# Optimization experiments

Measured on AMD Instinct MI355X. Metric: run time of the kernel, lower is better.

The kernel has to match this reference:

```python
import jax, jax.numpy as jnp
import numpy as np
import math

B, D, NH, NS, NT = 16, 256, 512, 8, 32
NV = NS * NT          # 256 prediction variables
L, H, A = 4, 8, 64    # attention layers, heads, head dim
HA = H * A            # 512
M = 512               # mlp_dim
R = 128               # resolution
EPS = 1e-5


def setup_inputs() -> dict:
    key = jax.random.key(0)
    ks = jax.random.split(key, 32)
    s = 0.02
    inp = {
        'hist_encoded': jax.random.normal(ks[0], (B, NH, D), jnp.float32),
        'hist_true_u': jax.random.uniform(ks[1], (B, NH), jnp.float32),
        'pred_encoded': jax.random.normal(ks[2], (B, NV, D), jnp.float32),
        'pred_true_u': jax.random.uniform(ks[3], (B, NV), jnp.float32),
        # dimension shifting layer
        'ds_w': jax.random.normal(ks[4], (D, HA), jnp.float32) * s,
        'ds_b': jnp.zeros((HA,), jnp.float32),
        # per-layer, per-head key/value creators: Linear(D+1 -> A)
        'key_w': jax.random.normal(ks[5], (L, H, D + 1, A), jnp.float32) * s,
        'key_b': jnp.zeros((L, H, A), jnp.float32),
        'val_w': jax.random.normal(ks[6], (L, H, D + 1, A), jnp.float32) * s,
        'val_b': jnp.zeros((L, H, A), jnp.float32),
        # layer norms
        'ln1_g': jnp.ones((L, HA), jnp.float32),
        'ln1_b': jnp.zeros((L, HA), jnp.float32),
        'ln2_g': jnp.ones((L, HA), jnp.float32),
        'ln2_b': jnp.zeros((L, HA), jnp.float32),
        # feed-forward (mlp_layers=2): HA->M, M->M, M->HA
        'ff_w1': jax.random.normal(ks[7], (L, HA, M), jnp.float32) * s,
        'ff_b1': jnp.zeros((L, M), jnp.float32),
        'ff_w2': jax.random.normal(ks[8], (L, M, M), jnp.float32) * s,
        'ff_b2': jnp.zeros((L, M), jnp.float32),
        'ff_w3': jax.random.normal(ks[9], (L, M, HA), jnp.float32) * s,
        'ff_b3': jnp.zeros((L, HA), jnp.float32),
        # dist extractor
        'de_w': jax.random.normal(ks[10], (HA, R), jnp.float32) * s,
        'de_b': jnp.zeros((R,), jnp.float32),
        'num_series': NS,
        'num_timesteps': NT,
    }
    return inp


def _ln(x, g, b):
    m = x.mean(-1, keepdims=True)
    v = ((x - m) ** 2).mean(-1, keepdims=True)
    return g * (x - m) / jnp.sqrt(v + EPS) + b


def _forward(hist_encoded, hist_true_u, pred_encoded, pred_true_u,
             ds_w, ds_b, key_w, key_b, val_w, val_b,
             ln1_g, ln1_b, ln2_g, ln2_b,
             ff_w1, ff_b1, ff_w2, ff_b2, ff_w3, ff_b3,
             de_w, de_b):
    Bm, NVm, Dm = pred_encoded.shape
    NHm = hist_encoded.shape[1]
    Lm, Hm, _, Am = key_w.shape
    W = NHm + NVm
    # identity permutation in the source loss() -> no-op
    att = pred_encoded @ ds_w + ds_b  # [B, NV, HA]
    # key/value inputs: [hist||u ; pred||u] -> [B, W, D+1]
    ki = jnp.concatenate([
        jnp.concatenate([hist_encoded, hist_true_u[:, :, None]], axis=2),
        jnp.concatenate([pred_encoded, pred_true_u[:, :, None]], axis=2)], axis=1)
    keys = jnp.einsum('bwd,lhda->lbhwa', ki, key_w) + key_b[:, None, :, None, :]
    vals = jnp.einsum('bwd,lhda->lbhwa', ki, val_w) + val_b[:, None, :, None, :]
    # flipped-triangular mask: position w is masked iff w >= NH + v
    mask = jnp.arange(W)[None, :] >= (NHm + jnp.arange(NVm)[:, None])  # [NV, W]
    scale = Am ** (-0.5)
    for l in range(Lm):
        avh = att.reshape(Bm, NVm, Hm, Am)
        prod = jnp.einsum('bvhi,bhwi->bhvw', avh, keys[l])  # [B,H,NV,W]
        prod = jnp.where(mask, -jnp.inf, prod) * scale
        w = jax.nn.softmax(prod, axis=-1)
        a = jnp.einsum('bhvw,bhwj->bvhj', w, vals[l]).reshape(Bm, NVm, Hm * Am)
        att = _ln(att + a, ln1_g[l], ln1_b[l])
        ff = jnp.maximum(att @ ff_w1[l] + ff_b1[l], 0.0)
        ff = jnp.maximum(ff @ ff_w2[l] + ff_b2[l], 0.0)
        ff = ff @ ff_w3[l] + ff_b3[l]
        att = _ln(att + ff, ln2_g[l], ln2_b[l])
    res = de_w.shape[-1]
    target = jnp.clip(jnp.floor(pred_true_u[:, 1:] * res).astype(jnp.int32), 0, res - 1)
    logits = (att @ de_w + de_b)[:, 1:, :]
    lp = math.log(res) + jax.nn.log_softmax(logits, axis=2)
    lp = jnp.take_along_axis(lp, target[:, :, None], axis=2)[:, :, 0]
    return -lp.sum(axis=1)  # [B]


def reference(hist_encoded, hist_true_u, pred_encoded, pred_true_u,
              ds_w, ds_b, key_w, key_b, val_w, val_b,
              ln1_g, ln1_b, ln2_g, ln2_b,
              ff_w1, ff_b1, ff_w2, ff_b2, ff_w3, ff_b3,
              de_w, de_b, num_series, num_timesteps):
    assert pred_encoded.shape[1] == num_series * num_timesteps
    return _forward(hist_encoded, hist_true_u, pred_encoded, pred_true_u,
                    ds_w, ds_b, key_w, key_b, val_w, val_b,
                    ln1_g, ln1_b, ln2_g, ln2_b,
                    ff_w1, ff_b1, ff_w2, ff_b2, ff_w3, ff_b3,
                    de_w, de_b)
```

## Files before the change

### kernel.cpp

```cpp
#include <hip/hip_runtime.h>

constexpr int kB = 16, kD = 256, kNH = 512, kNV = 256, kW = 768;
constexpr int kL = 4, kH = 8, kA = 64, kHA = 512, kM = 512, kR = 128;
constexpr int kKP = 288;
constexpr int kRows = kB * kNV;

typedef __bf16 bf16x8 __attribute__((ext_vector_type(8)));
typedef __bf16 bf16x4 __attribute__((ext_vector_type(4)));
typedef float f32x4 __attribute__((ext_vector_type(4)));

__device__ inline void load_lds16(const __bf16* g, __bf16* l) {
  __builtin_amdgcn_global_load_lds(
      (const __attribute__((address_space(1))) void*)g,
      (__attribute__((address_space(3))) void*)l, 16, 0, 0);
}

constexpr int kP1 = kB * kW * kKP;
constexpr int kPrepBlocks = 17681;

__global__ void prep_kernel(const float* __restrict__ hist,
                            const float* __restrict__ hist_u,
                            const float* __restrict__ pred,
                            const float* __restrict__ pred_u,
                            const float* __restrict__ kw,
                            const float* __restrict__ vw,
                            const float* __restrict__ w1,
                            const float* __restrict__ w2,
                            const float* __restrict__ w3,
                            const float* __restrict__ ds_w,
                            const float* __restrict__ de_w,
                            const float* __restrict__ key_b,
                            const float* __restrict__ val_b,
                            __bf16* __restrict__ ki,
                            __bf16* __restrict__ kvwt,
                            __bf16* __restrict__ ffwt,
                            __bf16* __restrict__ ds_wt,
                            __bf16* __restrict__ de_wt,
                            float* __restrict__ kvb,
                            float* __restrict__ outz) {
  __shared__ float ld[2080];
  const int bid = blockIdx.x;
  const int t = threadIdx.x;
  if (bid < 13824) {
    int i = bid * 256 + t;
    int d = i % kKP;
    int bw = i / kKP;
    int w = bw % kW;
    int b = bw / kW;
    float v = 0.f;
    if (d < 257) {
      if (w < kNH)
        v = (d < kD) ? hist[((size_t)b * kNH + w) * kD + d] : hist_u[b * kNH + w];
      else {
        int p = w - kNH;
        v = (d < kD) ? pred[((size_t)b * kNV + p) * kD + d] : pred_u[b * kNV + p];
      }
    }
    ki[i] = (__bf16)v;
  } else if (bid < 14400) {
    int bb = bid - 13824;
    bool isv = bb >= 288;
    int rem = isv ? bb - 288 : bb;
    int pair = rem / 9;
    int dt = rem - pair * 9;
    int d0 = dt * 32;
    const float* src = (isv ? vw : kw) + (size_t)pair * 257 * 64;
    int a = t & 63, dg = t >> 6;
#pragma unroll
    for (int ii = 0; ii < 8; ++ii) {
      int d = d0 + dg * 8 + ii;
      ld[(dg * 8 + ii) * 65 + a] = (d < 257) ? src[(size_t)d * 64 + a] : 0.f;
    }
    __syncthreads();
    int r = t >> 2, seg = t & 3;
    bf16x8 v;
#pragma unroll
    for (int j = 0; j < 8; ++j) v[j] = (__bf16)ld[(seg * 8 + j) * 65 + r];
    *(bf16x8*)&kvwt[((size_t)(isv ? 2048 : 0) + pair * 64 + r) * 288 + d0 +
                    seg * 8] = v;
  } else if (bid < 17472) {
    int cc = bid - 14400;
    int mat = cc >> 8;
    int tile = cc & 255;
    int n0 = (tile & 15) * 32, k0 = (tile >> 4) * 32;
    int l = mat / 3, which = mat - l * 3;
    const float* src = (which == 0 ? w1 : which == 1 ? w2 : w3) +
                       (size_t)l * 262144;
    int col = t & 31, kr = t >> 5;
#pragma unroll
    for (int p = 0; p < 4; ++p)
      ld[(kr + p * 8) * 33 + col] = src[(size_t)(k0 + kr + p * 8) * 512 + n0 + col];
    __syncthreads();
    int nr = t >> 3, seg = t & 7;
    bf16x4 v;
#pragma unroll
    for (int j = 0; j < 4; ++j) v[j] = (__bf16)ld[(seg * 4 + j) * 33 + nr];
    *(bf16x4*)&ffwt[(size_t)mat * 262144 + (n0 + nr) * 512 + k0 + seg * 4] = v;
  } else if (bid < 17600) {
    int cc = bid - 17472;
    int n0 = (cc & 15) * 32, k0 = (cc >> 4) * 32;
    int col = t & 31, kr = t >> 5;
#pragma unroll
    for (int p = 0; p < 4; ++p)
      ld[(kr + p * 8) * 33 + col] = ds_w[(size_t)(k0 + kr + p * 8) * 512 + n0 + col];
    __syncthreads();
    int nr = t >> 3, seg = t & 7;
    bf16x4 v;
#pragma unroll
    for (int j = 0; j < 4; ++j) v[j] = (__bf16)ld[(seg * 4 + j) * 33 + nr];
    *(bf16x4*)&ds_wt[(n0 + nr) * 256 + k0 + seg * 4] = v;
  } else if (bid < 17664) {
    int cc = bid - 17600;
    int n0 = (cc & 3) * 32, k0 = (cc >> 2) * 32;
    int col = t & 31, kr = t >> 5;
#pragma unroll
    for (int p = 0; p < 4; ++p)
      ld[(kr + p * 8) * 33 + col] = de_w[(size_t)(k0 + kr + p * 8) * 128 + n0 + col];
    __syncthreads();
    int nr = t >> 3, seg = t & 7;
    bf16x4 v;
#pragma unroll
    for (int j = 0; j < 4; ++j) v[j] = (__bf16)ld[(seg * 4 + j) * 33 + nr];
    *(bf16x4*)&de_wt[(n0 + nr) * 512 + k0 + seg * 4] = v;
  } else {
    int j = (bid - 17664) * 256 + t;
    if (j < 4096) {
      bool isv = j >= 2048;
      int cc = isv ? j - 2048 : j;
      int l = cc >> 9, rest = cc & 511;
      kvb[j] = isv ? val_b[l * 512 + rest] : key_b[l * 512 + rest];
    } else if (j < 4112) {
      outz[j - 4096] = 0.f;
    }
  }
}

template <int BN, int OMODE, bool RELU, bool KIMAP, bool BIASROW, int DEPTH>
__device__ __forceinline__ void gemm_core(
    int bxv, int byv, const __bf16* __restrict__ A,
    const __bf16* __restrict__ Bt, const float* __restrict__ bias,
    void* __restrict__ Cout, __bf16* __restrict__ Cout2, int K, int lda,
    int ldc, __bf16* Sm) {
  constexpr int JN = BN / 32;
  constexpr int BROWS = BN / 4;
  constexpr int SSTEP = (128 + BN) * 32;
  constexpr int LPS = (BN == 128) ? 4 : 3;
  constexpr int AH = DEPTH - 1;
  const int t = threadIdx.x;
  const int wid = t >> 6;
  const int lane = t & 63;
  const int bm = byv * 128;
  const int bn = bxv * BN;
  const int wm = (wid >> 1) * 64;
  const int wn = (wid & 1) * (BN / 2);
  const int sr = lane >> 2, sc = lane & 3;
  const int skey = (sr >> 1) & 3;
  const int abase = KIMAP ? ((bm >> 8) * 768 + 512 + (bm & 255)) : bm;
  const __bf16* Ag = A + (size_t)(abase + wid * 32 + sr) * lda + (sc ^ skey) * 8;
  const __bf16* Bg = Bt + (size_t)(bn + wid * BROWS + sr) * K + (sc ^ skey) * 8;

  auto stage = [&](int k0, __bf16* buf) {
    __bf16* As = buf;
    __bf16* Bs = buf + 4096;
    load_lds16(Ag + k0, As + (wid * 32) * 32);
    load_lds16(Ag + (size_t)16 * lda + k0, As + (wid * 32 + 16) * 32);
    load_lds16(Bg + k0, Bs + (wid * BROWS) * 32);
    if (BN == 128)
      load_lds16(Bg + (size_t)16 * K + k0, Bs + (wid * BROWS + 16) * 32);
  };

  f32x4 acc[4][JN] = {};
  const int q = lane >> 4, mr = lane & 15;
  const int rkey = (mr >> 1) & 3;
  const int nst = K >> 5;
  __bf16* b0 = Sm;
  __bf16* b1 = Sm + SSTEP;
  __bf16* b2 = Sm + 2 * SSTEP;
  __bf16* b3 = (DEPTH == 4) ? Sm + 3 * SSTEP : nullptr;
  stage(0, b0);
  stage(32, b1);
  if constexpr (DEPTH == 4) stage(64, b2);
  asm volatile("s_waitcnt vmcnt(%0)" ::"n"((AH - 1) * LPS) : "memory");
  __builtin_amdgcn_s_barrier();
  for (int k = 0; k < nst; ++k) {
    if (k + AH < nst) {
// ... 40 lines not shown
          float v = acc[i][j][r] +
                    (BIASROW ? bias[bm + wm + i * 16 + q * 4 + r] : bscol);
          if (RELU) v = fmaxf(v, 0.f);
          Cs[(wm + i * 16 + q * 4 + r) * PS + wn + j * 16 + mr] = (__bf16)v;
        }
      }
    }
    __syncthreads();
    constexpr int lpr = BN / 8;
    constexpr int rpi = 512 / BN;
    const int rl = lane / lpr, cl = (lane % lpr) * 8;
#pragma unroll
    for (int it = 0; it < BN / 16; ++it) {
      int row = wid * 32 + it * rpi + rl;
      bf16x8 v = *(const bf16x8*)&Cs[row * PS + cl];
      *(bf16x8*)((__bf16*)Cout + (size_t)(bm + row) * ldc + bn + cl) = v;
    }
  } else {
    constexpr int PSF = BN + 4;
    float* Csf = (float*)Sm;
#pragma unroll
    for (int j = 0; j < JN; ++j) {
      float bscol = bias[bn + wn + j * 16 + mr];
#pragma unroll
      for (int i = 0; i < 4; ++i) {
#pragma unroll
        for (int r = 0; r < 4; ++r) {
          float v = acc[i][j][r] + bscol;
          if (RELU) v = fmaxf(v, 0.f);
          Csf[(wm + i * 16 + q * 4 + r) * PSF + wn + j * 16 + mr] = v;
        }
      }
    }
    __syncthreads();
    const int rl = lane >> 4, cl = (lane & 15) * 4;
#pragma unroll
    for (int it = 0; it < 8; ++it) {
      int row = wid * 32 + it * 4 + rl;
      f32x4 v = *(const f32x4*)&Csf[row * PSF + cl];
      size_t gidx = (size_t)(bm + row) * ldc + bn + cl;
      *(f32x4*)((float*)Cout + gidx) = v;
      bf16x4 vb = {(__bf16)v[0], (__bf16)v[1], (__bf16)v[2], (__bf16)v[3]};
      *(bf16x4*)(Cout2 + gidx) = vb;
    }
  }
}

__global__ __launch_bounds__(256) void gemm3_kernel(
    const __bf16* __restrict__ ki, const __bf16* __restrict__ ds_wt,
    const float* __restrict__ ds_b, float* __restrict__ att,
    __bf16* __restrict__ att_bf, const __bf16* __restrict__ kv_wt,
    const float* __restrict__ kvb, __bf16* __restrict__ kvs_k,
    __bf16* __restrict__ vT) {
  __shared__ __bf16 smem[24576];
  int bid = blockIdx.x;
  if (bid < 256) {
    gemm_core<64, 2, false, true, false, 3>(bid & 7, bid >> 3, ki, ds_wt, ds_b,
                                            att, att_bf, 256, kKP, 512, smem);
  } else if (bid < 1792) {
    int b2 = bid - 256;
    gemm_core<128, 1, false, false, false, 3>(b2 & 15, b2 >> 4, ki, kv_wt, kvb,
                                              kvs_k, nullptr, kKP, kKP, 2048,
                                              smem);
  } else {
    int b3 = bid - 1792;
    gemm_core<128, 1, false, false, true, 3>(b3 % 96, b3 / 96,
                                             kv_wt + (size_t)2048 * kKP, ki,
                                             kvb + 2048, vT, nullptr, kKP, kKP,
                                             12288, smem);
  }
}

template <bool RELU>
__global__ __launch_bounds__(256) void gemm_ff_kernel(
    const __bf16* __restrict__ A, const __bf16* __restrict__ Bt,
    const float* __restrict__ bias, __bf16* __restrict__ Cout) {
  __shared__ __bf16 smem[24576];
  gemm_core<64, 1, RELU, false, false, 4>(blockIdx.x, blockIdx.y, A, Bt, bias,
                                          Cout, nullptr, 512, 512, 512, smem);
}

__global__ __launch_bounds__(256) void attn_mfma_kernel(
    const __bf16* __restrict__ attbf, const __bf16* __restrict__ kvs_k,
    const __bf16* __restrict__ vT, __bf16* __restrict__ outbf, int l) {
  const int id = blockIdx.x;
  const int kk = id >> 3;
  const int b = ((kk >> 5) << 3) | (id & 7);
  const int qt = kk & 3;
  const int h = (kk >> 2) & 7;
  __shared__ __bf16 Ks[64 * 72];
  __shared__ __bf16 Vt[64 * 72];
  __shared__ __bf16 Ps[64 * 72];
  const int t = threadIdx.x;
  const int w = t >> 6, lane = t & 63;
  const int quad = lane >> 4, mr = lane & 15;
  bf16x8 aq[2];
  {
    const __bf16* qp = attbf + ((size_t)(b * kNV + qt * 64 + w * 16 + mr) * kHA +
                                h * kA + quad * 8);
    aq[0] = *(const bf16x8*)qp;
    aq[1] = *(const bf16x8*)(qp + 32);
  }
  f32x4 o[4] = {};
  float m_ = -1e30f, l_ = 0.f;
  const int cmax = kNH + qt * 64;
  const int pr = t >> 2, pc = t & 3;
  const __bf16* kbase = kvs_k + ((size_t)(b * kW + pr) * 2048 + l * 512 + h * kA);
  const __bf16* vbase = vT + (size_t)(l * 512 + h * kA + pr) * 12288 + b * kW;
  bf16x8 kc0, kc1, vc0, vc1;
  kc0 = *(const bf16x8*)(kbase + pc * 8);
  kc1 = *(const bf16x8*)(kbase + pc * 8 + 32);
  vc0 = *(const bf16x8*)(vbase + pc * 16);
  vc1 = *(const bf16x8*)(vbase + pc * 16 + 8);
  for (int c0 = 0; c0 <= cmax; c0 += 64) {
    __syncthreads();
    *(bf16x8*)&Ks[pr * 72 + pc * 8] = kc0;
    *(bf16x8*)&Ks[pr * 72 + pc * 8 + 32] = kc1;
    *(bf16x8*)&Vt[pr * 72 + pc * 16] = vc0;
    *(bf16x8*)&Vt[pr * 72 + pc * 16 + 8] = vc1;
    __syncthreads();
    if (c0 + 64 <= cmax) {
      const __bf16* kp = kbase + (size_t)(c0 + 64) * 2048;
      const __bf16* vp = vbase + c0 + 64;
      kc0 = *(const bf16x8*)(kp + pc * 8);
      kc1 = *(const bf16x8*)(kp + pc * 8 + 32);
      vc0 = *(const bf16x8*)(vp + pc * 16);
      vc1 = *(const bf16x8*)(vp + pc * 16 + 8);
    }
    f32x4 s[4];
#pragma unroll
    for (int j = 0; j < 4; ++j) {
      bf16x8 ak0 = *(const bf16x8*)&Ks[(j * 16 + mr) * 72 + quad * 8];
      bf16x8 ak1 = *(const bf16x8*)&Ks[(j * 16 + mr) * 72 + quad * 8 + 32];
      f32x4 z = {};
      z = __builtin_amdgcn_mfma_f32_16x16x32_bf16(ak0, aq[0], z, 0, 0, 0);
      z = __builtin_amdgcn_mfma_f32_16x16x32_bf16(ak1, aq[1], z, 0, 0, 0);
      s[j] = z;
    }
    const int lim = cmax - c0;
    float sv[16], mx = -1e30f;
#pragma unroll
    for (int j = 0; j < 4; ++j)
#pragma unroll
      for (int r = 0; r < 4; ++r) {
        int p = j * 16 + quad * 4 + r;
        float x = (p < lim + mr) ? s[j][r] * 0.125f : -1e30f;
        sv[j * 4 + r] = x;
        mx = fmaxf(mx, x);
      }
    mx = fmaxf(mx, __shfl_xor(mx, 16));
    mx = fmaxf(mx, __shfl_xor(mx, 32));
    float mnew = fmaxf(m_, mx);
    float corr = __expf(m_ - mnew);
    float rs = 0.f;
#pragma unroll
    for (int i = 0; i < 16; ++i) {
      sv[i] = __expf(sv[i] - mnew);
      rs += sv[i];
    }
    rs += __shfl_xor(rs, 16);
    rs += __shfl_xor(rs, 32);
    l_ = l_ * corr + rs;
    m_ = mnew;
#pragma unroll
    for (int j = 0; j < 4; ++j) {
      bf16x4 pk = {(__bf16)sv[j * 4 + 0], (__bf16)sv[j * 4 + 1],
                   (__bf16)sv[j * 4 + 2], (__bf16)sv[j * 4 + 3]};
      *(bf16x4*)&Ps[(w * 16 + mr) * 72 + j * 16 + quad * 4] = pk;
    }
#pragma unroll
    for (int r = 0; r < 4; ++r) {
      float cr = __shfl(corr, quad * 4 + r);
#pragma unroll
      for (int j = 0; j < 4; ++j) o[j][r] *= cr;
    }
    bf16x8 ap0 = *(const bf16x8*)&Ps[(w * 16 + mr) * 72 + quad * 8];
    bf16x8 ap1 = *(const bf16x8*)&Ps[(w * 16 + mr) * 72 + quad * 8 + 32];
#pragma unroll
    for (int j = 0; j < 4; ++j) {
      bf16x8 b0 = *(const bf16x8*)&Vt[(j * 16 + mr) * 72 + quad * 8];
      bf16x8 b1 = *(const bf16x8*)&Vt[(j * 16 + mr) * 72 + quad * 8 + 32];
      o[j] = __builtin_amdgcn_mfma_f32_16x16x32_bf16(ap0, b0, o[j], 0, 0, 0);
      o[j] = __builtin_amdgcn_mfma_f32_16x16x32_bf16(ap1, b1, o[j], 0, 0, 0);
    }
  }
  float invl = 1.f / l_;
#pragma unroll
  for (int r = 0; r < 4; ++r) {
    float ir = __shfl(invl, quad * 4 + r);
    int row = b * kNV + qt * 64 + w * 16 + quad * 4 + r;
#pragma unroll
    for (int j = 0; j < 4; ++j)
      outbf[(size_t)row * kHA + h * kA + j * 16 + mr] = (__bf16)(o[j][r] * ir);
  }
}

__global__ __launch_bounds__(256) void add_ln_kernel(
    float* __restrict__ att, const __bf16* __restrict__ addbf,
    const float* __restrict__ g, const float* __restrict__ be,
    __bf16* __restrict__ attbf) {
  const int w = threadIdx.x >> 6, lane = threadIdx.x & 63;
  const int row = blockIdx.x * 4 + w;
  const int c0 = lane * 8;
  const size_t base = (size_t)row * kHA + c0;
  float4 a0 = *(const float4*)(att + base);
  float4 a1 = *(const float4*)(att + base + 4);
  bf16x8 dv = *(const bf16x8*)(addbf + base);
  float x[8] = {a0.x + (float)dv[0], a0.y + (float)dv[1], a0.z + (float)dv[2],
                a0.w + (float)dv[3], a1.x + (float)dv[4], a1.y + (float)dv[5],
                a1.z + (float)dv[6], a1.w + (float)dv[7]};
  float s = 0.f, q = 0.f;
#pragma unroll
  for (int j = 0; j < 8; ++j) { s += x[j]; q += x[j] * x[j]; }
#pragma unroll
  for (int o = 1; o < 64; o <<= 1) {
    s += __shfl_xor(s, o);
    q += __shfl_xor(q, o);
  }
  const float mean = s * (1.f / kHA);
  const float inv = rsqrtf(q * (1.f / kHA) - mean * mean + 1e-5f);
  float4 g0 = *(const float4*)(g + c0);
  float4 g1 = *(const float4*)(g + c0 + 4);
  float4 e0 = *(const float4*)(be + c0);
  float4 e1 = *(const float4*)(be + c0 + 4);
  float y[8];
  y[0] = g0.x * (x[0] - mean) * inv + e0.x;
  y[1] = g0.y * (x[1] - mean) * inv + e0.y;
  y[2] = g0.z * (x[2] - mean) * inv + e0.z;
  y[3] = g0.w * (x[3] - mean) * inv + e0.w;
  y[4] = g1.x * (x[4] - mean) * inv + e1.x;
  y[5] = g1.y * (x[5] - mean) * inv + e1.y;
  y[6] = g1.z * (x[6] - mean) * inv + e1.z;
  y[7] = g1.w * (x[7] - mean) * inv + e1.w;
  *(float4*)(att + base) = (float4){y[0], y[1], y[2], y[3]};
  *(float4*)(att + base + 4) = (float4){y[4], y[5], y[6], y[7]};
  bf16x8 yb = {(__bf16)y[0], (__bf16)y[1], (__bf16)y[2], (__bf16)y[3],
               (__bf16)y[4], (__bf16)y[5], (__bf16)y[6], (__bf16)y[7]};
  *(bf16x8*)(attbf + base) = yb;
}

__global__ __launch_bounds__(256) void de_loss_kernel(
    const float* __restrict__ att, const __bf16* __restrict__ fbf,
    const float* __restrict__ g2, const float* __restrict__ b2,
    const __bf16* __restrict__ de_wt, const float* __restrict__ de_b,
    const float* __restrict__ pred_u, float* __restrict__ out) {
  __shared__ __bf16 Als[64 * 512];
  __shared__ float red[4];
  const int blk = blockIdx.x;
  const int t = threadIdx.x;
  const int w = t >> 6, lane = t & 63, quad = lane >> 4, mr = lane & 15;
  {
    const int c0 = lane * 8;
    float4 ga = *(const float4*)(g2 + c0);
    float4 gb = *(const float4*)(g2 + c0 + 4);
    float4 ba = *(const float4*)(b2 + c0);
    float4 bb = *(const float4*)(b2 + c0 + 4);
    for (int rr = 0; rr < 16; ++rr) {
      const int lrow = w * 16 + rr;
      const size_t base = (size_t)(blk * 64 + lrow) * 512 + c0;
      float4 a0 = *(const float4*)(att + base);
      float4 a1 = *(const float4*)(att + base + 4);
      bf16x8 dv = *(const bf16x8*)(fbf + base);
      float x[8] = {a0.x + (float)dv[0], a0.y + (float)dv[1],
                    a0.z + (float)dv[2], a0.w + (float)dv[3],
                    a1.x + (float)dv[4], a1.y + (float)dv[5],
                    a1.z + (float)dv[6], a1.w + (float)dv[7]};
      float s = 0.f, q = 0.f;
#pragma unroll
      for (int j = 0; j < 8; ++j) { s += x[j]; q += x[j] * x[j]; }
#pragma unroll
      for (int o = 1; o < 64; o <<= 1) {
        s += __shfl_xor(s, o);
        q += __shfl_xor(q, o);
      }
      const float mean = s * (1.f / kHA);
      const float inv = rsqrtf(q * (1.f / kHA) - mean * mean + 1e-5f);
      bf16x8 yv = {(__bf16)(ga.x * (x[0] - mean) * inv + ba.x),
                   (__bf16)(ga.y * (x[1] - mean) * inv + ba.y),
                   (__bf16)(ga.z * (x[2] - mean) * inv + ba.z),
                   (__bf16)(ga.w * (x[3] - mean) * inv + ba.w),
                   (__bf16)(gb.x * (x[4] - mean) * inv + bb.x),
                   (__bf16)(gb.y * (x[5] - mean) * inv + bb.y),
                   (__bf16)(gb.z * (x[6] - mean) * inv + bb.z),
                   (__bf16)(gb.w * (x[7] - mean) * inv + bb.w)};
      *(bf16x8*)&Als[lrow * 512 + ((lane ^ (lrow & 7)) << 3)] = yv;
    }
  }
  __syncthreads();
  const int row0 = blk * 64 + w * 16;
  const int lrowA = w * 16 + mr;
  f32x4 acc[8] = {};
#pragma unroll 4
  for (int k0 = 0; k0 < 512; k0 += 32) {
    const int grp = (((k0 >> 3) + quad) ^ (lrowA & 7)) << 3;
    bf16x8 a = *(const bf16x8*)&Als[lrowA * 512 + grp];
#pragma unroll
    for (int j = 0; j < 8; ++j) {
      bf16x8 bb =
          *(const bf16x8*)(de_wt + (size_t)(j * 16 + mr) * 512 + k0 + quad * 8);
      acc[j] = __builtin_amdgcn_mfma_f32_16x16x32_bf16(a, bb, acc[j], 0, 0, 0);
    }
  }
  float dbv[8];
#pragma unroll
  for (int j = 0; j < 8; ++j) dbv[j] = de_b[j * 16 + mr];
  float lpacc = 0.f;
#pragma unroll
  for (int r = 0; r < 4; ++r) {
    int row = row0 + quad * 4 + r;
    int v = row & 255;
    float lg[8], mx = -1e30f;
#pragma unroll
    for (int j = 0; j < 8; ++j) {
      lg[j] = acc[j][r] + dbv[j];
// ... 19 lines not shown
    cand += __shfl_xor(cand, 2);
    cand += __shfl_xor(cand, 4);
    cand += __shfl_xor(cand, 8);
    float lp = (v >= 1) ? (4.8520302639196171f + cand - lse) : 0.f;
    lpacc += lp;
  }
  lpacc += __shfl_xor(lpacc, 16);
  lpacc += __shfl_xor(lpacc, 32);
  if (lane == 0) red[w] = lpacc;
  __syncthreads();
  if (t == 0)
    atomicAdd(&out[blk >> 2], -(red[0] + red[1] + red[2] + red[3]));
}

extern "C" void kernel_launch(void* const* d_in, const int* in_sizes, int n_in,
                              void* d_out, int out_size, void* d_ws, size_t ws_size,
                              hipStream_t stream) {
  const float* hist   = (const float*)d_in[0];
  const float* hist_u = (const float*)d_in[1];
  const float* pred   = (const float*)d_in[2];
  const float* pred_u = (const float*)d_in[3];
  const float* ds_w   = (const float*)d_in[4];
  const float* ds_b   = (const float*)d_in[5];
  const float* key_w  = (const float*)d_in[6];
  const float* key_b  = (const float*)d_in[7];
  const float* val_w  = (const float*)d_in[8];
  const float* val_b  = (const float*)d_in[9];
  const float* ln1_g  = (const float*)d_in[10];
  const float* ln1_b  = (const float*)d_in[11];
  const float* ln2_g  = (const float*)d_in[12];
  const float* ln2_b  = (const float*)d_in[13];
  const float* ff_w1  = (const float*)d_in[14];
  const float* ff_b1  = (const float*)d_in[15];
  const float* ff_w2  = (const float*)d_in[16];
  const float* ff_b2  = (const float*)d_in[17];
  const float* ff_w3  = (const float*)d_in[18];
  const float* ff_b3  = (const float*)d_in[19];
  const float* de_w   = (const float*)d_in[20];
  const float* de_b   = (const float*)d_in[21];
  float* out = (float*)d_out;

  char* ws = (char*)d_ws;
  size_t off = 0;
  auto alloc = [&](size_t bytes) { char* p = ws + off; off += bytes; return p; };
  __bf16* ki_bf  = (__bf16*)alloc((size_t)kB * kW * kKP * 2);
  __bf16* kv_wt  = (__bf16*)alloc((size_t)4096 * kKP * 2);
  __bf16* ffw_t  = (__bf16*)alloc((size_t)12 * 512 * 512 * 2);
  __bf16* ds_wt  = (__bf16*)alloc((size_t)512 * 256 * 2);
  __bf16* de_wt  = (__bf16*)alloc((size_t)128 * 512 * 2);
  float*  kvb    = (float*)alloc((size_t)4096 * 4);
  __bf16* kvs_k  = (__bf16*)alloc((size_t)kB * kW * 2048 * 2);
  __bf16* vT     = (__bf16*)alloc((size_t)2048 * 12288 * 2);
  float*  att    = (float*)alloc((size_t)kRows * kHA * 4);
  __bf16* att_bf = (__bf16*)alloc((size_t)kRows * kHA * 2);
  __bf16* tmp_bf = (__bf16*)alloc((size_t)kRows * kHA * 2);
  __bf16* ff1_bf = (__bf16*)alloc((size_t)kRows * kM * 2);
  __bf16* ff2_bf = (__bf16*)alloc((size_t)kRows * kM * 2);

  prep_kernel<<<kPrepBlocks, 256, 0, stream>>>(
      hist, hist_u, pred, pred_u, key_w, val_w, ff_w1, ff_w2, ff_w3, ds_w, de_w,
      key_b, val_b, ki_bf, kv_wt, ffw_t, ds_wt, de_wt, kvb, out);

  gemm3_kernel<<<3328, 256, 0, stream>>>(ki_bf, ds_wt, ds_b, att, att_bf, kv_wt,
                                         kvb, kvs_k, vT);

  for (int l = 0; l < kL; ++l) {
    attn_mfma_kernel<<<512, 256, 0, stream>>>(att_bf, kvs_k, vT, tmp_bf, l);
    add_ln_kernel<<<kRows / 4, 256, 0, stream>>>(att, tmp_bf, ln1_g + l * kHA,
                                                 ln1_b + l * kHA, att_bf);
    gemm_ff_kernel<true><<<dim3(kM / 64, kRows / 128), 256, 0, stream>>>(
        att_bf, ffw_t + (size_t)(l * 3) * 262144, ff_b1 + l * kM, ff1_bf);
    gemm_ff_kernel<true><<<dim3(kM / 64, kRows / 128), 256, 0, stream>>>(
        ff1_bf, ffw_t + (size_t)(l * 3 + 1) * 262144, ff_b2 + l * kM, ff2_bf);
    gemm_ff_kernel<false><<<dim3(kHA / 64, kRows / 128), 256, 0, stream>>>(
        ff2_bf, ffw_t + (size_t)(l * 3 + 2) * 262144, ff_b3 + l * kHA, tmp_bf);
    if (l < kL - 1)
      add_ln_kernel<<<kRows / 4, 256, 0, stream>>>(att, tmp_bf,
                                                   ln2_g + l * kHA,
                                                   ln2_b + l * kHA, att_bf);
  }
  de_loss_kernel<<<64, 256, 0, stream>>>(att, tmp_bf, ln2_g + 3 * kHA,
                                         ln2_b + 3 * kHA, de_wt, de_b, pred_u,
                                         out);
}
```

Measured before the change: 413.3 us.

## Fuse per-layer LN and three FF GEMMs into one kernel with panel flags

Replaces the per-layer sequence of add_ln, three FF GEMM launches and a second add_ln with a single 256-block kernel. Blocks working on the same 128-row panel coordinate through per-phase atomic counters instead of kernel boundaries. This is meant to remove four launch gaps and the full-device drains between them per layer, and to let different panels proceed independently. It relies on all 256 blocks being co-resident, otherwise the spin-waits could deadlock. Each GEMM phase now uses only 256 blocks, so there may be less parallelism per phase than before.

```diff
diff --git a/kernel.cpp b/kernel.cpp
--- a/kernel.cpp
+++ b/kernel.cpp
@@ -16,7 +16,7 @@
 }
 
 constexpr int kP1 = kB * kW * kKP;
-constexpr int kPrepBlocks = 17681;
+constexpr int kPrepBlocks = 17683;
 
 __global__ void prep_kernel(const float* __restrict__ hist,
                             const float* __restrict__ hist_u,
@@ -37,7 +37,8 @@
                             __bf16* __restrict__ ds_wt,
                             __bf16* __restrict__ de_wt,
                             float* __restrict__ kvb,
-                            float* __restrict__ outz) {
+                            float* __restrict__ outz,
+                            int* __restrict__ flagsz) {
   __shared__ float ld[2080];
   const int bid = blockIdx.x;
   const int t = threadIdx.x;
@@ -131,6 +132,8 @@
       kvb[j] = isv ? val_b[l * 512 + rest] : key_b[l * 512 + rest];
     } else if (j < 4112) {
       outz[j - 4096] = 0.f;
+    } else if (j < 4624) {
+      flagsz[j - 4112] = 0;
     }
   }
 }
@@ -296,13 +299,100 @@
   }
 }
 
-template <bool RELU>
-__global__ __launch_bounds__(256) void gemm_ff_kernel(
-    const __bf16* __restrict__ A, const __bf16* __restrict__ Bt,
-    const float* __restrict__ bias, __bf16* __restrict__ Cout) {
+__device__ __forceinline__ void ln_rows16(
+    float* __restrict__ att, const __bf16* __restrict__ addbf,
+    const float* __restrict__ g, const float* __restrict__ be,
+    __bf16* __restrict__ attbf, int row0, int w, int lane) {
+  const int c0 = lane * 8;
+  float4 g0 = *(const float4*)(g + c0);
+  float4 g1 = *(const float4*)(g + c0 + 4);
+  float4 e0 = *(const float4*)(be + c0);
+  float4 e1 = *(const float4*)(be + c0 + 4);
+#pragma unroll
+  for (int it = 0; it < 4; ++it) {
+    const int row = row0 + it * 4 + w;
+    const size_t base = (size_t)row * kHA + c0;
+    float4 a0 = *(const float4*)(att + base);
+    float4 a1 = *(const float4*)(att + base + 4);
+    bf16x8 dv = *(const bf16x8*)(addbf + base);
+    float x[8] = {a0.x + (float)dv[0], a0.y + (float)dv[1], a0.z + (float)dv[2],
+                  a0.w + (float)dv[3], a1.x + (float)dv[4], a1.y + (float)dv[5],
+                  a1.z + (float)dv[6], a1.w + (float)dv[7]};
+    float s = 0.f, q = 0.f;
+#pragma unroll
+    for (int j = 0; j < 8; ++j) { s += x[j]; q += x[j] * x[j]; }
+#pragma unroll
+    for (int o = 1; o < 64; o <<= 1) {
+      s += __shfl_xor(s, o);
+      q += __shfl_xor(q, o);
+    }
+    const float mean = s * (1.f / kHA);
+    const float inv = rsqrtf(q * (1.f / kHA) - mean * mean + 1e-5f);
+    float y[8];
+    y[0] = g0.x * (x[0] - mean) * inv + e0.x;
+    y[1] = g0.y * (x[1] - mean) * inv + e0.y;
+    y[2] = g0.z * (x[2] - mean) * inv + e0.z;
+    y[3] = g0.w * (x[3] - mean) * inv + e0.w;
+    y[4] = g1.x * (x[4] - mean) * inv + e1.x;
+    y[5] = g1.y * (x[5] - mean) * inv + e1.y;
+    y[6] = g1.z * (x[6] - mean) * inv + e1.z;
+    y[7] = g1.w * (x[7] - mean) * inv + e1.w;
+    *(float4*)(att + base) = (float4){y[0], y[1], y[2], y[3]};
+    *(float4*)(att + base + 4) = (float4){y[4], y[5], y[6], y[7]};
+    bf16x8 yb = {(__bf16)y[0], (__bf16)y[1], (__bf16)y[2], (__bf16)y[3],
+                 (__bf16)y[4], (__bf16)y[5], (__bf16)y[6], (__bf16)y[7]};
+    *(bf16x8*)(attbf + base) = yb;
+  }
+}
+
+__global__ __launch_bounds__(256) void layer_ff_kernel(
+    float* __restrict__ att, const __bf16* __restrict__ atmp,
+    const float* __restrict__ g1v, const float* __restrict__ b1v,
+    const float* __restrict__ g2v, const float* __restrict__ b2v,
+    const __bf16* __restrict__ Wt, const float* __restrict__ fb1,
+    const float* __restrict__ fb2, const float* __restrict__ fb3,
+    __bf16* __restrict__ attbf, __bf16* __restrict__ f1,
+    __bf16* __restrict__ f2, __bf16* __restrict__ f3,
+    int* __restrict__ flags, int skip_ln2) {
   __shared__ __bf16 smem[24576];
-  gemm_core<64, 1, RELU, false, false, 4>(blockIdx.x, blockIdx.y, A, Bt, bias,
-                                          Cout, nullptr, 512, 512, 512, smem);
+  const int id = blockIdx.x;
+  const int tid = threadIdx.x;
+  const int w = tid >> 6, lane = tid & 63;
+  const int panel = id >> 3, bx = id & 7;
+
+  auto release = [&](int phase) {
+    __threadfence();
+    __syncthreads();
+    if (tid == 0)
+      __hip_atomic_fetch_add(&flags[phase * 32 + panel], 1, __ATOMIC_RELEASE,
+                             __HIP_MEMORY_SCOPE_AGENT);
+  };
+  auto acquire = [&](int phase) {
+    if (tid == 0)
+      while (__hip_atomic_load(&flags[phase * 32 + panel], __ATOMIC_ACQUIRE,
+                               __HIP_MEMORY_SCOPE_AGENT) < 8)
+        __builtin_amdgcn_s_sleep(2);
+    __syncthreads();
+  };
+
+  ln_rows16(att, atmp, g1v, b1v, attbf, id * 16, w, lane);
+  release(0);
+  acquire(0);
+  gemm_core<64, 1, true, false, false, 4>(bx, panel, attbf, Wt, fb1, f1,
+                                          nullptr, 512, 512, 512, smem);
+  release(1);
+  acquire(1);
+  gemm_core<64, 1, true, false, false, 4>(bx, panel, f1, Wt + 262144, fb2, f2,
+                                          nullptr, 512, 512, 512, smem);
+  release(2);
+  acquire(2);
+  gemm_core<64, 1, false, false, false, 4>(bx, panel, f2, Wt + 524288, fb3, f3,
+                                           nullptr, 512, 512, 512, smem);
+  release(3);
+  if (!skip_ln2) {
+    acquire(3);
+    ln_rows16(att, f3, g2v, b2v, attbf, id * 16, w, lane);
+  }
 }
 
 __global__ __launch_bounds__(256) void attn_mfma_kernel(
@@ -418,50 +508,6 @@
     for (int j = 0; j < 4; ++j)
       outbf[(size_t)row * kHA + h * kA + j * 16 + mr] = (__bf16)(o[j][r] * ir);
   }
-}
-
-__global__ __launch_bounds__(256) void add_ln_kernel(
-    float* __restrict__ att, const __bf16* __restrict__ addbf,
-    const float* __restrict__ g, const float* __restrict__ be,
-    __bf16* __restrict__ attbf) {
-  const int w = threadIdx.x >> 6, lane = threadIdx.x & 63;
-  const int row = blockIdx.x * 4 + w;
-  const int c0 = lane * 8;
-  const size_t base = (size_t)row * kHA + c0;
-  float4 a0 = *(const float4*)(att + base);
-  float4 a1 = *(const float4*)(att + base + 4);
-  bf16x8 dv = *(const bf16x8*)(addbf + base);
-  float x[8] = {a0.x + (float)dv[0], a0.y + (float)dv[1], a0.z + (float)dv[2],
-                a0.w + (float)dv[3], a1.x + (float)dv[4], a1.y + (float)dv[5],
-                a1.z + (float)dv[6], a1.w + (float)dv[7]};
-  float s = 0.f, q = 0.f;
-#pragma unroll
-  for (int j = 0; j < 8; ++j) { s += x[j]; q += x[j] * x[j]; }
-#pragma unroll
-  for (int o = 1; o < 64; o <<= 1) {
-    s += __shfl_xor(s, o);
-    q += __shfl_xor(q, o);
-  }
-  const float mean = s * (1.f / kHA);
-  const float inv = rsqrtf(q * (1.f / kHA) - mean * mean + 1e-5f);
-  float4 g0 = *(const float4*)(g + c0);
-  float4 g1 = *(const float4*)(g + c0 + 4);
-  float4 e0 = *(const float4*)(be + c0);
-  float4 e1 = *(const float4*)(be + c0 + 4);
-  float y[8];
-  y[0] = g0.x * (x[0] - mean) * inv + e0.x;
-  y[1] = g0.y * (x[1] - mean) * inv + e0.y;
-  y[2] = g0.z * (x[2] - mean) * inv + e0.z;
-  y[3] = g0.w * (x[3] - mean) * inv + e0.w;
-  y[4] = g1.x * (x[4] - mean) * inv + e1.x;
-  y[5] = g1.y * (x[5] - mean) * inv + e1.y;
-  y[6] = g1.z * (x[6] - mean) * inv + e1.z;
-  y[7] = g1.w * (x[7] - mean) * inv + e1.w;
-  *(float4*)(att + base) = (float4){y[0], y[1], y[2], y[3]};
-  *(float4*)(att + base + 4) = (float4){y[4], y[5], y[6], y[7]};
-  bf16x8 yb = {(__bf16)y[0], (__bf16)y[1], (__bf16)y[2], (__bf16)y[3],
-               (__bf16)y[4], (__bf16)y[5], (__bf16)y[6], (__bf16)y[7]};
-  *(bf16x8*)(attbf + base) = yb;
 }
 
 __global__ __launch_bounds__(256) void de_loss_kernel(
@@ -614,28 +660,22 @@
   __bf16* tmp_bf = (__bf16*)alloc((size_t)kRows * kHA * 2);
   __bf16* ff1_bf = (__bf16*)alloc((size_t)kRows * kM * 2);
   __bf16* ff2_bf = (__bf16*)alloc((size_t)kRows * kM * 2);
+  int*    flags  = (int*)alloc((size_t)512 * 4);
 
   prep_kernel<<<kPrepBlocks, 256, 0, stream>>>(
       hist, hist_u, pred, pred_u, key_w, val_w, ff_w1, ff_w2, ff_w3, ds_w, de_w,
-      key_b, val_b, ki_bf, kv_wt, ffw_t, ds_wt, de_wt, kvb, out);
+      key_b, val_b, ki_bf, kv_wt, ffw_t, ds_wt, de_wt, kvb, out, flags);
 
   gemm3_kernel<<<3328, 256, 0, stream>>>(ki_bf, ds_wt, ds_b, att, att_bf, kv_wt,
                                          kvb, kvs_k, vT);
 
   for (int l = 0; l < kL; ++l) {
     attn_mfma_kernel<<<512, 256, 0, stream>>>(att_bf, kvs_k, vT, tmp_bf, l);
-    add_ln_kernel<<<kRows / 4, 256, 0, stream>>>(att, tmp_bf, ln1_g + l * kHA,
-                                                 ln1_b + l * kHA, att_bf);
-    gemm_ff_kernel<true><<<dim3(kM / 64, kRows / 128), 256, 0, stream>>>(
-        att_bf, ffw_t + (size_t)(l * 3) * 262144, ff_b1 + l * kM, ff1_bf);
-    gemm_ff_kernel<true><<<dim3(kM / 64, kRows / 128), 256, 0, stream>>>(
-        ff1_bf, ffw_t + (size_t)(l * 3 + 1) * 262144, ff_b2 + l * kM, ff2_bf);
-    gemm_ff_kernel<false><<<dim3(kHA / 64, kRows / 128), 256, 0, stream>>>(
-        ff2_bf, ffw_t + (size_t)(l * 3 + 2) * 262144, ff_b3 + l * kHA, tmp_bf);
-    if (l < kL - 1)
-      add_ln_kernel<<<kRows / 4, 256, 0, stream>>>(att, tmp_bf,
-                                                   ln2_g + l * kHA,
-                                                   ln2_b + l * kHA, att_bf);
+    layer_ff_kernel<<<256, 256, 0, stream>>>(
+        att, tmp_bf, ln1_g + l * kHA, ln1_b + l * kHA, ln2_g + l * kHA,
+        ln2_b + l * kHA, ffw_t + (size_t)(l * 3) * 262144, ff_b1 + l * kM,
+        ff_b2 + l * kM, ff_b3 + l * kHA, att_bf, ff1_bf, ff2_bf, tmp_bf,
+        flags + l * 128, l == kL - 1);
   }
   de_loss_kernel<<<64, 256, 0, stream>>>(att, tmp_bf, ln2_g + 3 * kHA,
                                          ln2_b + 3 * kHA, de_wt, de_b, pred_u,
```

New measurement: 1.015 ms. +145.6%, slower.

## Fuse first add+LayerNorm into the FF1 GEMM via a separate fp32 residual buffer

Applied to the files above, without the earlier changes.

Replaces the post-attention add_ln kernel and the first FF GEMM with one kernel. Each block computes the LayerNorm of 64 rows directly into swizzled LDS and then runs a 64x128 MFMA GEMM over the full K=512, staging B tiles with global_load_lds triple buffering. A new y32 buffer holds the fp32 post-LN1 residual, written only by the bx==0 blocks, and the second add-LN and the loss kernel read from it. This removes one launch and the bf16 activation round trip. In exchange each row group's LayerNorm is recomputed four times, and the grid is only 256 blocks.

```diff
diff --git a/kernel.cpp b/kernel.cpp
--- a/kernel.cpp
+++ b/kernel.cpp
@@ -305,6 +305,120 @@
                                           Cout, nullptr, 512, 512, 512, smem);
 }
 
+__global__ __launch_bounds__(256) void ff1_fused_kernel(
+    const float* __restrict__ att, const __bf16* __restrict__ atmp,
+    const float* __restrict__ g1, const float* __restrict__ b1g,
+    const __bf16* __restrict__ Wt, const float* __restrict__ fb1,
+    float* __restrict__ y32, __bf16* __restrict__ f1) {
+  __shared__ __bf16 Als[64 * 512];
+  __shared__ __bf16 Bsm[3 * 4096];
+  const int id = blockIdx.x;
+  const int rg = id >> 2, bx = id & 3;
+  const int tid = threadIdx.x;
+  const int w = tid >> 6, lane = tid & 63;
+  const int quad = lane >> 4, mr = lane & 15;
+  {
+    const int c0 = lane * 8;
+    float4 ga = *(const float4*)(g1 + c0);
+    float4 gb = *(const float4*)(g1 + c0 + 4);
+    float4 ba = *(const float4*)(b1g + c0);
+    float4 bb = *(const float4*)(b1g + c0 + 4);
+    for (int it = 0; it < 16; ++it) {
+      const int lrow = it * 4 + w;
+      const size_t base = (size_t)(rg * 64 + lrow) * 512 + c0;
+      float4 a0 = *(const float4*)(att + base);
+      float4 a1 = *(const float4*)(att + base + 4);
+      bf16x8 dv = *(const bf16x8*)(atmp + base);
+      float x[8] = {a0.x + (float)dv[0], a0.y + (float)dv[1],
+                    a0.z + (float)dv[2], a0.w + (float)dv[3],
+                    a1.x + (float)dv[4], a1.y + (float)dv[5],
+                    a1.z + (float)dv[6], a1.w + (float)dv[7]};
+      float s = 0.f, q = 0.f;
+#pragma unroll
+      for (int j = 0; j < 8; ++j) { s += x[j]; q += x[j] * x[j]; }
+#pragma unroll
+      for (int o = 1; o < 64; o <<= 1) {
+        s += __shfl_xor(s, o);
+        q += __shfl_xor(q, o);
+      }
+      const float mean = s * (1.f / kHA);
+      const float inv = rsqrtf(q * (1.f / kHA) - mean * mean + 1e-5f);
+      float y[8];
+      y[0] = ga.x * (x[0] - mean) * inv + ba.x;
+      y[1] = ga.y * (x[1] - mean) * inv + ba.y;
+      y[2] = ga.z * (x[2] - mean) * inv + ba.z;
+      y[3] = ga.w * (x[3] - mean) * inv + ba.w;
+      y[4] = gb.x * (x[4] - mean) * inv + bb.x;
+      y[5] = gb.y * (x[5] - mean) * inv + bb.y;
+      y[6] = gb.z * (x[6] - mean) * inv + bb.z;
+      y[7] = gb.w * (x[7] - mean) * inv + bb.w;
+      bf16x8 yv = {(__bf16)y[0], (__bf16)y[1], (__bf16)y[2], (__bf16)y[3],
+                   (__bf16)y[4], (__bf16)y[5], (__bf16)y[6], (__bf16)y[7]};
+      *(bf16x8*)&Als[lrow * 512 + ((lane ^ (lrow & 7)) << 3)] = yv;
+      if (bx == 0) {
+        *(float4*)(y32 + base) = (float4){y[0], y[1], y[2], y[3]};
+        *(float4*)(y32 + base + 4) = (float4){y[4], y[5], y[6], y[7]};
+      }
+    }
+  }
+  __syncthreads();
+  const int sr = lane >> 2, sc = lane & 3;
+  const int skey = (sr >> 1) & 3;
+  const __bf16* Bg =
+      Wt + (size_t)(bx * 128 + w * 32 + sr) * 512 + (sc ^ skey) * 8;
+  auto stageB = [&](int k0, __bf16* Bs) {
+    load_lds16(Bg + k0, Bs + (w * 32) * 32);
+    load_lds16(Bg + (size_t)16 * 512 + k0, Bs + (w * 32 + 16) * 32);
+  };
+  const int rkey = (mr >> 1) & 3;
+  const int arow = w * 16 + mr;
+  f32x4 acc[8] = {};
+  __bf16* p0 = Bsm;
+  __bf16* p1 = Bsm + 4096;
+  __bf16* p2 = Bsm + 8192;
+  stageB(0, p0);
+  stageB(32, p1);
+  asm volatile("s_waitcnt vmcnt(2)" ::: "memory");
+  __builtin_amdgcn_s_barrier();
+  for (int k = 0; k < 16; ++k) {
+    if (k + 2 < 16) stageB((k + 2) << 5, p2);
+    const int grp = (((k << 2) + quad) ^ (mr & 7)) << 3;
+    bf16x8 af = *(const bf16x8*)&Als[arow * 512 + grp];
+    bf16x8 bfr[8];
+#pragma unroll
+    for (int j = 0; j < 8; ++j)
+      bfr[j] = *(const bf16x8*)(p0 + (j * 16 + mr) * 32 + (quad ^ rkey) * 8);
+#pragma unroll
+    for (int j = 0; j < 8; ++j)
+      acc[j] = __builtin_amdgcn_mfma_f32_16x16x32_bf16(af, bfr[j], acc[j], 0,
+                                                       0, 0);
+    if (k + 3 <= 16)
+      asm volatile("s_waitcnt vmcnt(2)" ::: "memory");
+    else
+      asm volatile("s_waitcnt vmcnt(0)" ::: "memory");
+    __builtin_amdgcn_s_barrier();
+    __bf16* tp = p0; p0 = p1; p1 = p2; p2 = tp;
+  }
+  __bf16* Cs = Bsm;
+#pragma unroll
+  for (int j = 0; j < 8; ++j) {
+    float bc = fb1[bx * 128 + j * 16 + mr];
+#pragma unroll
+    for (int r = 0; r < 4; ++r) {
+      float v = fmaxf(acc[j][r] + bc, 0.f);
+      Cs[(w * 16 + quad * 4 + r) * 136 + j * 16 + mr] = (__bf16)v;
+    }
+  }
+  __syncthreads();
+#pragma unroll
+  for (int p = 0; p < 4; ++p) {
+    int row_l = w * 16 + p * 4 + (lane >> 4);
+    int col_l = (lane & 15) * 8;
+    bf16x8 v = *(const bf16x8*)&Cs[row_l * 136 + col_l];
+    *(bf16x8*)&f1[(size_t)(rg * 64 + row_l) * 512 + bx * 128 + col_l] = v;
+  }
+}
+
 __global__ __launch_bounds__(256) void attn_mfma_kernel(
     const __bf16* __restrict__ attbf, const __bf16* __restrict__ kvs_k,
     const __bf16* __restrict__ vT, __bf16* __restrict__ outbf, int l) {
@@ -420,17 +534,17 @@
   }
 }
 
-__global__ __launch_bounds__(256) void add_ln_kernel(
-    float* __restrict__ att, const __bf16* __restrict__ addbf,
-    const float* __restrict__ g, const float* __restrict__ be,
-    __bf16* __restrict__ attbf) {
+__global__ __launch_bounds__(256) void add_ln2_kernel(
+    float* __restrict__ att, const float* __restrict__ y32,
+    const __bf16* __restrict__ f3, const float* __restrict__ g,
+    const float* __restrict__ be, __bf16* __restrict__ attbf) {
   const int w = threadIdx.x >> 6, lane = threadIdx.x & 63;
   const int row = blockIdx.x * 4 + w;
   const int c0 = lane * 8;
   const size_t base = (size_t)row * kHA + c0;
-  float4 a0 = *(const float4*)(att + base);
-  float4 a1 = *(const float4*)(att + base + 4);
-  bf16x8 dv = *(const bf16x8*)(addbf + base);
+  float4 a0 = *(const float4*)(y32 + base);
+  float4 a1 = *(const float4*)(y32 + base + 4);
+  bf16x8 dv = *(const bf16x8*)(f3 + base);
   float x[8] = {a0.x + (float)dv[0], a0.y + (float)dv[1], a0.z + (float)dv[2],
                 a0.w + (float)dv[3], a1.x + (float)dv[4], a1.y + (float)dv[5],
                 a1.z + (float)dv[6], a1.w + (float)dv[7]};
@@ -465,7 +579,7 @@
 }
 
 __global__ __launch_bounds__(256) void de_loss_kernel(
-    const float* __restrict__ att, const __bf16* __restrict__ fbf,
+    const float* __restrict__ y32, const __bf16* __restrict__ fbf,
     const float* __restrict__ g2, const float* __restrict__ b2,
     const __bf16* __restrict__ de_wt, const float* __restrict__ de_b,
     const float* __restrict__ pred_u, float* __restrict__ out) {
@@ -483,8 +597,8 @@
     for (int rr = 0; rr < 16; ++rr) {
       const int lrow = w * 16 + rr;
       const size_t base = (size_t)(blk * 64 + lrow) * 512 + c0;
-      float4 a0 = *(const float4*)(att + base);
-      float4 a1 = *(const float4*)(att + base + 4);
+      float4 a0 = *(const float4*)(y32 + base);
+      float4 a1 = *(const float4*)(y32 + base + 4);
       bf16x8 dv = *(const bf16x8*)(fbf + base);
       float x[8] = {a0.x + (float)dv[0], a0.y + (float)dv[1],
                     a0.z + (float)dv[2], a0.w + (float)dv[3],
@@ -610,6 +724,7 @@
   __bf16* kvs_k  = (__bf16*)alloc((size_t)kB * kW * 2048 * 2);
   __bf16* vT     = (__bf16*)alloc((size_t)2048 * 12288 * 2);
   float*  att    = (float*)alloc((size_t)kRows * kHA * 4);
+  float*  y32    = (float*)alloc((size_t)kRows * kHA * 4);
   __bf16* att_bf = (__bf16*)alloc((size_t)kRows * kHA * 2);
   __bf16* tmp_bf = (__bf16*)alloc((size_t)kRows * kHA * 2);
   __bf16* ff1_bf = (__bf16*)alloc((size_t)kRows * kM * 2);
@@ -624,20 +739,18 @@
 
   for (int l = 0; l < kL; ++l) {
     attn_mfma_kernel<<<512, 256, 0, stream>>>(att_bf, kvs_k, vT, tmp_bf, l);
-    add_ln_kernel<<<kRows / 4, 256, 0, stream>>>(att, tmp_bf, ln1_g + l * kHA,
-                                                 ln1_b + l * kHA, att_bf);
-    gemm_ff_kernel<true><<<dim3(kM / 64, kRows / 128), 256, 0, stream>>>(
-        att_bf, ffw_t + (size_t)(l * 3) * 262144, ff_b1 + l * kM, ff1_bf);
+    ff1_fused_kernel<<<256, 256, 0, stream>>>(
+        att, tmp_bf, ln1_g + l * kHA, ln1_b + l * kHA,
+        ffw_t + (size_t)(l * 3) * 262144, ff_b1 + l * kM, y32, ff1_bf);
     gemm_ff_kernel<true><<<dim3(kM / 64, kRows / 128), 256, 0, stream>>>(
         ff1_bf, ffw_t + (size_t)(l * 3 + 1) * 262144, ff_b2 + l * kM, ff2_bf);
     gemm_ff_kernel<false><<<dim3(kHA / 64, kRows / 128), 256, 0, stream>>>(
         ff2_bf, ffw_t + (size_t)(l * 3 + 2) * 262144, ff_b3 + l * kHA, tmp_bf);
     if (l < kL - 1)
-      add_ln_kernel<<<kRows / 4, 256, 0, stream>>>(att, tmp_bf,
-                                                   ln2_g + l * kHA,
-                                                   ln2_b + l * kHA, att_bf);
-  }
-  de_loss_kernel<<<64, 256, 0, stream>>>(att, tmp_bf, ln2_g + 3 * kHA,
+      add_ln2_kernel<<<kRows / 4, 256, 0, stream>>>(
+          att, y32, tmp_bf, ln2_g + l * kHA, ln2_b + l * kHA, att_bf);
+  }
+  de_loss_kernel<<<64, 256, 0, stream>>>(y32, tmp_bf, ln2_g + 3 * kHA,
                                          ln2_b + 3 * kHA, de_wt, de_b, pred_u,
                                          out);
 }
```

Measured after the change: 445.4 us. +7.8%, slower.

## Double-buffer attention K/V tiles, vectorize input prep, deepen KV GEMM pipeline

Applied to the files above, without the earlier changes.

The attention kernel now keeps two LDS buffers for K and V and writes the next tile during the current iteration, so each tile needs one barrier instead of two and the global loads are issued two tiles ahead. The prep kernel's input-packing section now has each thread produce two bf16 values with a single paired store, which halves that section's block count. The K/V projection GEMMs move from a pipeline depth of 3 to 4, which enlarges shared memory to 64 KB per block and may lower occupancy.

```diff
diff --git a/kernel.cpp b/kernel.cpp
--- a/kernel.cpp
+++ b/kernel.cpp
@@ -7,6 +7,7 @@
 
 typedef __bf16 bf16x8 __attribute__((ext_vector_type(8)));
 typedef __bf16 bf16x4 __attribute__((ext_vector_type(4)));
+typedef __bf16 bf16x2 __attribute__((ext_vector_type(2)));
 typedef float f32x4 __attribute__((ext_vector_type(4)));
 
 __device__ inline void load_lds16(const __bf16* g, __bf16* l) {
@@ -15,8 +16,7 @@
       (__attribute__((address_space(3))) void*)l, 16, 0, 0);
 }
 
-constexpr int kP1 = kB * kW * kKP;
-constexpr int kPrepBlocks = 17681;
+constexpr int kPrepBlocks = 10769;
 
 __global__ void prep_kernel(const float* __restrict__ hist,
                             const float* __restrict__ hist_u,
@@ -41,24 +41,32 @@
   __shared__ float ld[2080];
   const int bid = blockIdx.x;
   const int t = threadIdx.x;
-  if (bid < 13824) {
-    int i = bid * 256 + t;
-    int d = i % kKP;
-    int bw = i / kKP;
-    int w = bw % kW;
-    int b = bw / kW;
-    float v = 0.f;
-    if (d < 257) {
-      if (w < kNH)
-        v = (d < kD) ? hist[((size_t)b * kNH + w) * kD + d] : hist_u[b * kNH + w];
-      else {
-        int p = w - kNH;
-        v = (d < kD) ? pred[((size_t)b * kNV + p) * kD + d] : pred_u[b * kNV + p];
+  if (bid < 6912) {
+    int i = bid * 512 + t * 2;
+    __bf16 v2[2];
+#pragma unroll
+    for (int e = 0; e < 2; ++e) {
+      int ii = i + e;
+      int d = ii % kKP;
+      int bw = ii / kKP;
+      int w = bw % kW;
+      int b = bw / kW;
+      float v = 0.f;
+      if (d < 257) {
+        if (w < kNH)
+          v = (d < kD) ? hist[((size_t)b * kNH + w) * kD + d]
+                       : hist_u[b * kNH + w];
+        else {
+          int p = w - kNH;
+          v = (d < kD) ? pred[((size_t)b * kNV + p) * kD + d]
+                       : pred_u[b * kNV + p];
+        }
       }
-    }
-    ki[i] = (__bf16)v;
-  } else if (bid < 14400) {
-    int bb = bid - 13824;
+      v2[e] = (__bf16)v;
+    }
+    *(bf16x2*)&ki[i] = bf16x2{v2[0], v2[1]};
+  } else if (bid < 7488) {
+    int bb = bid - 6912;
     bool isv = bb >= 288;
     int rem = isv ? bb - 288 : bb;
     int pair = rem / 9;
@@ -78,8 +86,8 @@
     for (int j = 0; j < 8; ++j) v[j] = (__bf16)ld[(seg * 8 + j) * 65 + r];
     *(bf16x8*)&kvwt[((size_t)(isv ? 2048 : 0) + pair * 64 + r) * 288 + d0 +
                     seg * 8] = v;
-  } else if (bid < 17472) {
-    int cc = bid - 14400;
+  } else if (bid < 10560) {
+    int cc = bid - 7488;
     int mat = cc >> 8;
     int tile = cc & 255;
     int n0 = (tile & 15) * 32, k0 = (tile >> 4) * 32;
@@ -96,8 +104,8 @@
 #pragma unroll
     for (int j = 0; j < 4; ++j) v[j] = (__bf16)ld[(seg * 4 + j) * 33 + nr];
     *(bf16x4*)&ffwt[(size_t)mat * 262144 + (n0 + nr) * 512 + k0 + seg * 4] = v;
-  } else if (bid < 17600) {
-    int cc = bid - 17472;
+  } else if (bid < 10688) {
+    int cc = bid - 10560;
     int n0 = (cc & 15) * 32, k0 = (cc >> 4) * 32;
     int col = t & 31, kr = t >> 5;
 #pragma unroll
@@ -109,8 +117,8 @@
 #pragma unroll
     for (int j = 0; j < 4; ++j) v[j] = (__bf16)ld[(seg * 4 + j) * 33 + nr];
     *(bf16x4*)&ds_wt[(n0 + nr) * 256 + k0 + seg * 4] = v;
-  } else if (bid < 17664) {
-    int cc = bid - 17600;
+  } else if (bid < 10752) {
+    int cc = bid - 10688;
     int n0 = (cc & 3) * 32, k0 = (cc >> 2) * 32;
     int col = t & 31, kr = t >> 5;
 #pragma unroll
@@ -123,7 +131,7 @@
     for (int j = 0; j < 4; ++j) v[j] = (__bf16)ld[(seg * 4 + j) * 33 + nr];
     *(bf16x4*)&de_wt[(n0 + nr) * 512 + k0 + seg * 4] = v;
   } else {
-    int j = (bid - 17664) * 256 + t;
+    int j = (bid - 10752) * 256 + t;
     if (j < 4096) {
       bool isv = j >= 2048;
       int cc = isv ? j - 2048 : j;
@@ -277,19 +285,19 @@
     __bf16* __restrict__ att_bf, const __bf16* __restrict__ kv_wt,
     const float* __restrict__ kvb, __bf16* __restrict__ kvs_k,
     __bf16* __restrict__ vT) {
-  __shared__ __bf16 smem[24576];
+  __shared__ __bf16 smem[32768];
   int bid = blockIdx.x;
   if (bid < 256) {
     gemm_core<64, 2, false, true, false, 3>(bid & 7, bid >> 3, ki, ds_wt, ds_b,
                                             att, att_bf, 256, kKP, 512, smem);
   } else if (bid < 1792) {
     int b2 = bid - 256;
-    gemm_core<128, 1, false, false, false, 3>(b2 & 15, b2 >> 4, ki, kv_wt, kvb,
+    gemm_core<128, 1, false, false, false, 4>(b2 & 15, b2 >> 4, ki, kv_wt, kvb,
                                               kvs_k, nullptr, kKP, kKP, 2048,
                                               smem);
   } else {
     int b3 = bid - 1792;
-    gemm_core<128, 1, false, false, true, 3>(b3 % 96, b3 / 96,
+    gemm_core<128, 1, false, false, true, 4>(b3 % 96, b3 / 96,
                                              kv_wt + (size_t)2048 * kKP, ki,
                                              kvb + 2048, vT, nullptr, kKP, kKP,
                                              12288, smem);
@@ -313,8 +321,8 @@
   const int b = ((kk >> 5) << 3) | (id & 7);
   const int qt = kk & 3;
   const int h = (kk >> 2) & 7;
-  __shared__ __bf16 Ks[64 * 72];
-  __shared__ __bf16 Vt[64 * 72];
+  __shared__ __bf16 Ks[2][64 * 72];
+  __shared__ __bf16 Vt[2][64 * 72];
   __shared__ __bf16 Ps[64 * 72];
   const int t = threadIdx.x;
   const int w = t >> 6, lane = t & 63;
@@ -329,40 +337,42 @@
   f32x4 o[4] = {};
   float m_ = -1e30f, l_ = 0.f;
   const int cmax = kNH + qt * 64;
+  const int nt = (cmax >> 6) + 1;
   const int pr = t >> 2, pc = t & 3;
   const __bf16* kbase = kvs_k + ((size_t)(b * kW + pr) * 2048 + l * 512 + h * kA);
   const __bf16* vbase = vT + (size_t)(l * 512 + h * kA + pr) * 12288 + b * kW;
   bf16x8 kc0, kc1, vc0, vc1;
-  kc0 = *(const bf16x8*)(kbase + pc * 8);
-  kc1 = *(const bf16x8*)(kbase + pc * 8 + 32);
-  vc0 = *(const bf16x8*)(vbase + pc * 16);
-  vc1 = *(const bf16x8*)(vbase + pc * 16 + 8);
-  for (int c0 = 0; c0 <= cmax; c0 += 64) {
-    __syncthreads();
-    *(bf16x8*)&Ks[pr * 72 + pc * 8] = kc0;
-    *(bf16x8*)&Ks[pr * 72 + pc * 8 + 32] = kc1;
-    *(bf16x8*)&Vt[pr * 72 + pc * 16] = vc0;
-    *(bf16x8*)&Vt[pr * 72 + pc * 16 + 8] = vc1;
-    __syncthreads();
-    if (c0 + 64 <= cmax) {
-      const __bf16* kp = kbase + (size_t)(c0 + 64) * 2048;
-      const __bf16* vp = vbase + c0 + 64;
-      kc0 = *(const bf16x8*)(kp + pc * 8);
-      kc1 = *(const bf16x8*)(kp + pc * 8 + 32);
-      vc0 = *(const bf16x8*)(vp + pc * 16);
-      vc1 = *(const bf16x8*)(vp + pc * 16 + 8);
-    }
+  auto loadt = [&](int tt) {
+    const __bf16* kp = kbase + (size_t)(tt << 6) * 2048;
+    const __bf16* vp = vbase + (tt << 6);
+    kc0 = *(const bf16x8*)(kp + pc * 8);
+    kc1 = *(const bf16x8*)(kp + pc * 8 + 32);
+    vc0 = *(const bf16x8*)(vp + pc * 16);
+    vc1 = *(const bf16x8*)(vp + pc * 16 + 8);
+  };
+  auto writet = [&](int buf) {
+    *(bf16x8*)&Ks[buf][pr * 72 + pc * 8] = kc0;
+    *(bf16x8*)&Ks[buf][pr * 72 + pc * 8 + 32] = kc1;
+    *(bf16x8*)&Vt[buf][pr * 72 + pc * 16] = vc0;
+    *(bf16x8*)&Vt[buf][pr * 72 + pc * 16 + 8] = vc1;
+  };
+  loadt(0);
+  writet(0);
+  if (nt > 1) loadt(1);
+  __syncthreads();
+  for (int tt = 0; tt < nt; ++tt) {
+    const int cur = tt & 1;
     f32x4 s[4];
 #pragma unroll
     for (int j = 0; j < 4; ++j) {
-      bf16x8 ak0 = *(const bf16x8*)&Ks[(j * 16 + mr) * 72 + quad * 8];
-      bf16x8 ak1 = *(const bf16x8*)&Ks[(j * 16 + mr) * 72 + quad * 8 + 32];
+      bf16x8 ak0 = *(const bf16x8*)&Ks[cur][(j * 16 + mr) * 72 + quad * 8];
+      bf16x8 ak1 = *(const bf16x8*)&Ks[cur][(j * 16 + mr) * 72 + quad * 8 + 32];
       f32x4 z = {};
       z = __builtin_amdgcn_mfma_f32_16x16x32_bf16(ak0, aq[0], z, 0, 0, 0);
       z = __builtin_amdgcn_mfma_f32_16x16x32_bf16(ak1, aq[1], z, 0, 0, 0);
       s[j] = z;
     }
-    const int lim = cmax - c0;
+    const int lim = cmax - (tt << 6);
     float sv[16], mx = -1e30f;
 #pragma unroll
     for (int j = 0; j < 4; ++j)
@@ -403,10 +413,15 @@
     bf16x8 ap1 = *(const bf16x8*)&Ps[(w * 16 + mr) * 72 + quad * 8 + 32];
 #pragma unroll
     for (int j = 0; j < 4; ++j) {
-      bf16x8 b0 = *(const bf16x8*)&Vt[(j * 16 + mr) * 72 + quad * 8];
-      bf16x8 b1 = *(const bf16x8*)&Vt[(j * 16 + mr) * 72 + quad * 8 + 32];
+      bf16x8 b0 = *(const bf16x8*)&Vt[cur][(j * 16 + mr) * 72 + quad * 8];
+      bf16x8 b1 = *(const bf16x8*)&Vt[cur][(j * 16 + mr) * 72 + quad * 8 + 32];
       o[j] = __builtin_amdgcn_mfma_f32_16x16x32_bf16(ap0, b0, o[j], 0, 0, 0);
       o[j] = __builtin_amdgcn_mfma_f32_16x16x32_bf16(ap1, b1, o[j], 0, 0, 0);
+    }
+    if (tt + 1 < nt) {
+      writet(cur ^ 1);
+      if (tt + 2 < nt) loadt(tt + 2);
+      __syncthreads();
     }
   }
   float invl = 1.f / l_;
```

New measurement: 412.2 us. Within noise of the previous version (-0.3%).
